# Performance work log

Hardware: AMD Instinct MI355X
Metric: run time of the kernel (lower is better)

## Reference

```python
import jax, jax.numpy as jnp
import numpy as np

SHAPE = (64, 64, 64, 16)
RANK = 8


def tr_to_matrix(factors, in_dim):
    # Tensor-ring reconstruction: T[i1..id] = trace(G1[:,i1,:] @ ... @ Gd[:,id,:])
    acc = factors[0]  # (r, n0, r)
    for f in factors[1:]:
        r = acc.shape[0]
        acc = jnp.einsum('amb,bnc->amnc', acc, f).reshape(r, -1, r)
    # close the ring with a trace over the boundary rank
    full = jnp.trace(acc, axis1=0, axis2=2)  # (prod(SHAPE),)
    return full.reshape(in_dim, -1)


def setup_inputs() -> dict:
    key = jax.random.key(0)
    ks = jax.random.split(key, 5)
    x = jax.random.normal(ks[0], (8192, 2048), dtype=jnp.float32)
    factors = {}
    for i, n in enumerate(SHAPE):
        factors[f'f{i}'] = jax.random.uniform(
            ks[i + 1], (RANK, n, RANK), dtype=jnp.float32, minval=-0.1, maxval=0.1)
    return {'x': x, **factors}


def reference(x, f0, f1, f2, f3):
    W = tr_to_matrix([f0, f1, f2, f3], x.shape[1])  # (2048, 2048)
    return jnp.matmul(x, W)
```

## Files before the change

kernel.cpp:

```cpp
#include <hip/hip_runtime.h>
#include <hip/hip_bf16.h>
#include <stdint.h>

typedef unsigned short u16;
typedef __attribute__((ext_vector_type(8))) unsigned short u16x8;
typedef __attribute__((ext_vector_type(8))) __bf16 bf16x8;
typedef __attribute__((ext_vector_type(4))) float f32x4;

__device__ __forceinline__ u16 f2bf(float f) {
    uint32_t u = __builtin_bit_cast(uint32_t, f);
    u = (u + 0x7fffu + ((u >> 16) & 1u)) >> 16;
    return (u16)u;
}

__device__ __forceinline__ float bf2f(u16 v) {
    return __builtin_bit_cast(float, (uint32_t)v << 16);
}

__device__ __forceinline__ bf16x8 cvt8(const float* p) {
    f32x4 a = *(const f32x4*)p;
    f32x4 b = *(const f32x4*)(p + 4);
    u16x8 o;
    o[0] = f2bf(a[0]); o[1] = f2bf(a[1]); o[2] = f2bf(a[2]); o[3] = f2bf(a[3]);
    o[4] = f2bf(b[0]); o[5] = f2bf(b[1]); o[6] = f2bf(b[2]); o[7] = f2bf(b[3]);
    return __builtin_bit_cast(bf16x8, o);
}

__global__ __launch_bounds__(256) void prep_kernel(const float* __restrict__ f0,
                                                   const float* __restrict__ f1,
                                                   const float* __restrict__ f2,
                                                   const float* __restrict__ f3,
                                                   u16* __restrict__ H12bT,
                                                   u16* __restrict__ H34T) {
    int gid = blockIdx.x * 256 + threadIdx.x;
    if (gid < 262144) {
        int rc = gid >> 11;
        int k  = gid & 2047;
        int p = rc >> 6, e = rc & 63;
        int a = e >> 3, b = e & 7;
        int i1 = k >> 5, i2 = ((k & 31) << 1) | p;
        float s = 0.f;
#pragma unroll
        for (int m = 0; m < 8; m++)
            s += f0[a * 512 + i1 * 8 + m] * f1[m * 512 + i2 * 8 + b];
        H12bT[gid] = f2bf(s);
    } else {
        int g = gid - 262144;
        int c = g >> 6;
        int e = g & 63;
        int a = e >> 3, b = e & 7;
        int i3 = c >> 4, i4 = c & 15;
        float s = 0.f;
#pragma unroll
        for (int cc = 0; cc < 8; cc++)
            s += f2[b * 512 + i3 * 8 + cc] * f3[cc * 128 + i4 * 8 + a];
        H34T[c * 64 + e] = f2bf(s);
    }
}

__global__ __launch_bounds__(256) void k1_kernel(const float* __restrict__ x,
                                                 const u16* __restrict__ H12bT,
                                                 u16* __restrict__ Ypb) {
    int tid = threadIdx.x, lane = tid & 63, w = tid >> 6;
    int lm = lane & 15, lkE = (lane >> 4) << 3;
    int r0 = blockIdx.x * 128 + w * 32;
    int k0 = blockIdx.y * 256;

    f32x4 acc[2][8];
#pragma unroll
    for (int i = 0; i < 2; ++i)
#pragma unroll
        for (int j = 0; j < 8; ++j) acc[i][j] = (f32x4){0.f, 0.f, 0.f, 0.f};

    const float* xA0 = x + (size_t)(r0 + lm) * 2048 + k0 + lkE;
    const float* xA1 = xA0 + (size_t)16 * 2048;
    const u16*   bP  = H12bT + (size_t)lm * 2048 + k0 + lkE;

#pragma unroll
    for (int kc = 0; kc < 8; ++kc) {
        int ko = kc * 32;
        bf16x8 a0 = cvt8(xA0 + ko);
        bf16x8 a1 = cvt8(xA1 + ko);
        bf16x8 bf[8];
#pragma unroll
        for (int j = 0; j < 8; ++j)
            bf[j] = __builtin_bit_cast(bf16x8, *(const u16x8*)(bP + (size_t)j * 16 * 2048 + ko));
#pragma unroll
        for (int j = 0; j < 8; ++j) {
            acc[0][j] = __builtin_amdgcn_mfma_f32_16x16x32_bf16(a0, bf[j], acc[0][j], 0, 0, 0);
            acc[1][j] = __builtin_amdgcn_mfma_f32_16x16x32_bf16(a1, bf[j], acc[1][j], 0, 0, 0);
        }
    }
    u16* yw = Ypb + (size_t)blockIdx.y * 1048576 + (size_t)(r0 + ((lane >> 4) << 2)) * 128 + lm;
#pragma unroll
    for (int mi = 0; mi < 2; ++mi)
#pragma unroll
        for (int j = 0; j < 8; ++j) {
            f32x4 v = acc[mi][j];
#pragma unroll
            for (int r = 0; r < 4; ++r)
                yw[(size_t)(mi * 16 + r) * 128 + j * 16] = f2bf(v[r]);
        }
}

__global__ __launch_bounds__(256) void k2r_kernel(const u16* __restrict__ Ypb,
                                                  const u16* __restrict__ H34T,
                                                  float* __restrict__ out) {
    __shared__ u16 Yl[32][136];
    int tid = threadIdx.x, lane = tid & 63, w = tid >> 6;
    int lm = lane & 15, lkE = (lane >> 4) << 3;
    int r0 = blockIdx.x * 32;

    {
        int row0 = tid >> 4;
        int ce = (tid & 15) << 3;
        float s0[8], s1[8];
#pragma unroll
        for (int e = 0; e < 8; ++e) { s0[e] = 0.f; s1[e] = 0.f; }
#pragma unroll
        for (int ks = 0; ks < 8; ++ks) {
            const u16* b = Ypb + (size_t)ks * 1048576 + (size_t)r0 * 128;
            u16x8 v0 = *(const u16x8*)(b + (size_t)row0 * 128 + ce);
            u16x8 v1 = *(const u16x8*)(b + (size_t)(16 + row0) * 128 + ce);
#pragma unroll
            for (int e = 0; e < 8; ++e) { s0[e] += bf2f(v0[e]); s1[e] += bf2f(v1[e]); }
        }
        u16x8 o0, o1;
#pragma unroll
        for (int e = 0; e < 8; ++e) { o0[e] = f2bf(s0[e]); o1[e] = f2bf(s1[e]); }
        *(u16x8*)&Yl[row0][ce] = o0;
        *(u16x8*)&Yl[16 + row0][ce] = o1;
    }
    __syncthreads();

    int p = w >> 1, ch = (w & 1) << 9;
    bf16x8 ya[2][2];
#pragma unroll
    for (int rh = 0; rh < 2; ++rh)
#pragma unroll
        for (int kc = 0; kc < 2; ++kc)
            ya[rh][kc] = __builtin_bit_cast(bf16x8,
                *(const u16x8*)&Yl[rh * 16 + lm][p * 64 + kc * 32 + lkE]);

    const u16* hB = H34T + (size_t)(ch + lm) * 64 + lkE;
    float* cW = out + (size_t)(r0 + ((lane >> 4) << 2)) * 2048 + (w << 9) + lm;

#pragma unroll 4
    for (int cf = 0; cf < 32; ++cf) {
        const u16* hr = hB + (size_t)cf * 1024;
        bf16x8 h0 = __builtin_bit_cast(bf16x8, *(const u16x8*)(hr));
        bf16x8 h1 = __builtin_bit_cast(bf16x8, *(const u16x8*)(hr + 32));
        f32x4 a0 = (f32x4){0.f, 0.f, 0.f, 0.f};
        f32x4 a1 = (f32x4){0.f, 0.f, 0.f, 0.f};
        a0 = __builtin_amdgcn_mfma_f32_16x16x32_bf16(ya[0][0], h0, a0, 0, 0, 0);
        a0 = __builtin_amdgcn_mfma_f32_16x16x32_bf16(ya[0][1], h1, a0, 0, 0, 0);
        a1 = __builtin_amdgcn_mfma_f32_16x16x32_bf16(ya[1][0], h0, a1, 0, 0, 0);
        a1 = __builtin_amdgcn_mfma_f32_16x16x32_bf16(ya[1][1], h1, a1, 0, 0, 0);
#pragma unroll
        for (int r = 0; r < 4; ++r) {
            cW[(size_t)r * 2048 + cf * 16] = a0[r];
            cW[(size_t)(16 + r) * 2048 + cf * 16] = a1[r];
        }
    }
}

extern "C" void kernel_launch(void* const* d_in, const int* in_sizes, int n_in,
                              void* d_out, int out_size, void* d_ws, size_t ws_size,
                              hipStream_t stream) {
    const float* x  = (const float*)d_in[0];
    const float* f0 = (const float*)d_in[1];
    const float* f1 = (const float*)d_in[2];
    const float* f2 = (const float*)d_in[3];
    const float* f3 = (const float*)d_in[4];
    float* out = (float*)d_out;

    char* ws = (char*)d_ws;
    u16* H12bT = (u16*)ws;
    u16* H34T  = (u16*)(ws + (512u << 10));
    u16* Ypb   = (u16*)(ws + (1u << 20));
    if (ws_size < ((size_t)18 << 20)) return;

    prep_kernel<<<1280, 256, 0, stream>>>(f0, f1, f2, f3, H12bT, H34T);
    k1_kernel<<<dim3(64, 8), 256, 0, stream>>>(x, H12bT, Ypb);
    k2r_kernel<<<256, 256, 0, stream>>>(Ypb, H34T, out);
}
```

Before: 58.59 us.

## Halve per-wave work in k1 and double threads per block in k2r

k1 now gives each wave 16 rows instead of 32 and launches twice as many blocks, so there are more waves in flight to hide the latency of streaming x. k2r moves to 512-thread blocks: the reduction step loads one row per thread, and each wave covers 256 output columns instead of 512. The cost is less reuse, since each H12 B-fragment load in k1 now feeds one MFMA instead of two, which doubles B-operand traffic.

Result: slower. 66.77 us (+14.0%).

```diff
diff --git a/kernel.cpp b/kernel.cpp
--- a/kernel.cpp
+++ b/kernel.cpp
@@ -63,47 +63,39 @@
                                                  u16* __restrict__ Ypb) {
     int tid = threadIdx.x, lane = tid & 63, w = tid >> 6;
     int lm = lane & 15, lkE = (lane >> 4) << 3;
-    int r0 = blockIdx.x * 128 + w * 32;
+    int r0 = blockIdx.x * 64 + w * 16;
     int k0 = blockIdx.y * 256;
 
-    f32x4 acc[2][8];
+    f32x4 acc[8];
 #pragma unroll
-    for (int i = 0; i < 2; ++i)
-#pragma unroll
-        for (int j = 0; j < 8; ++j) acc[i][j] = (f32x4){0.f, 0.f, 0.f, 0.f};
+    for (int j = 0; j < 8; ++j) acc[j] = (f32x4){0.f, 0.f, 0.f, 0.f};
 
     const float* xA0 = x + (size_t)(r0 + lm) * 2048 + k0 + lkE;
-    const float* xA1 = xA0 + (size_t)16 * 2048;
     const u16*   bP  = H12bT + (size_t)lm * 2048 + k0 + lkE;
 
 #pragma unroll
     for (int kc = 0; kc < 8; ++kc) {
         int ko = kc * 32;
         bf16x8 a0 = cvt8(xA0 + ko);
-        bf16x8 a1 = cvt8(xA1 + ko);
         bf16x8 bf[8];
 #pragma unroll
         for (int j = 0; j < 8; ++j)
             bf[j] = __builtin_bit_cast(bf16x8, *(const u16x8*)(bP + (size_t)j * 16 * 2048 + ko));
 #pragma unroll
-        for (int j = 0; j < 8; ++j) {
-            acc[0][j] = __builtin_amdgcn_mfma_f32_16x16x32_bf16(a0, bf[j], acc[0][j], 0, 0, 0);
-            acc[1][j] = __builtin_amdgcn_mfma_f32_16x16x32_bf16(a1, bf[j], acc[1][j], 0, 0, 0);
-        }
+        for (int j = 0; j < 8; ++j)
+            acc[j] = __builtin_amdgcn_mfma_f32_16x16x32_bf16(a0, bf[j], acc[j], 0, 0, 0);
     }
     u16* yw = Ypb + (size_t)blockIdx.y * 1048576 + (size_t)(r0 + ((lane >> 4) << 2)) * 128 + lm;
 #pragma unroll
-    for (int mi = 0; mi < 2; ++mi)
+    for (int j = 0; j < 8; ++j) {
+        f32x4 v = acc[j];
 #pragma unroll
-        for (int j = 0; j < 8; ++j) {
-            f32x4 v = acc[mi][j];
-#pragma unroll
-            for (int r = 0; r < 4; ++r)
-                yw[(size_t)(mi * 16 + r) * 128 + j * 16] = f2bf(v[r]);
-        }
+        for (int r = 0; r < 4; ++r)
+            yw[(size_t)r * 128 + j * 16] = f2bf(v[r]);
+    }
 }
 
-__global__ __launch_bounds__(256) void k2r_kernel(const u16* __restrict__ Ypb,
+__global__ __launch_bounds__(512) void k2r_kernel(const u16* __restrict__ Ypb,
                                                   const u16* __restrict__ H34T,
                                                   float* __restrict__ out) {
     __shared__ u16 Yl[32][136];
@@ -114,26 +106,24 @@
     {
         int row0 = tid >> 4;
         int ce = (tid & 15) << 3;
-        float s0[8], s1[8];
+        float s0[8];
 #pragma unroll
-        for (int e = 0; e < 8; ++e) { s0[e] = 0.f; s1[e] = 0.f; }
+        for (int e = 0; e < 8; ++e) s0[e] = 0.f;
 #pragma unroll
         for (int ks = 0; ks < 8; ++ks) {
-            const u16* b = Ypb + (size_t)ks * 1048576 + (size_t)r0 * 128;
-            u16x8 v0 = *(const u16x8*)(b + (size_t)row0 * 128 + ce);
-            u16x8 v1 = *(const u16x8*)(b + (size_t)(16 + row0) * 128 + ce);
+            const u16* b = Ypb + (size_t)ks * 1048576 + (size_t)(r0 + row0) * 128 + ce;
+            u16x8 v = *(const u16x8*)b;
 #pragma unroll
-            for (int e = 0; e < 8; ++e) { s0[e] += bf2f(v0[e]); s1[e] += bf2f(v1[e]); }
+            for (int e = 0; e < 8; ++e) s0[e] += bf2f(v[e]);
         }
-        u16x8 o0, o1;
+        u16x8 o;
 #pragma unroll
-        for (int e = 0; e < 8; ++e) { o0[e] = f2bf(s0[e]); o1[e] = f2bf(s1[e]); }
-        *(u16x8*)&Yl[row0][ce] = o0;
-        *(u16x8*)&Yl[16 + row0][ce] = o1;
+        for (int e = 0; e < 8; ++e) o[e] = f2bf(s0[e]);
+        *(u16x8*)&Yl[row0][ce] = o;
     }
     __syncthreads();
 
-    int p = w >> 1, ch = (w & 1) << 9;
+    int p = w >> 2, ch = (w & 3) << 8;
     bf16x8 ya[2][2];
 #pragma unroll
     for (int rh = 0; rh < 2; ++rh)
@@ -143,10 +133,10 @@
                 *(const u16x8*)&Yl[rh * 16 + lm][p * 64 + kc * 32 + lkE]);
 
     const u16* hB = H34T + (size_t)(ch + lm) * 64 + lkE;
-    float* cW = out + (size_t)(r0 + ((lane >> 4) << 2)) * 2048 + (w << 9) + lm;
+    float* cW = out + (size_t)(r0 + ((lane >> 4) << 2)) * 2048 + (w << 8) + lm;
 
 #pragma unroll 4
-    for (int cf = 0; cf < 32; ++cf) {
+    for (int cf = 0; cf < 16; ++cf) {
         const u16* hr = hB + (size_t)cf * 1024;
         bf16x8 h0 = __builtin_bit_cast(bf16x8, *(const u16x8*)(hr));
         bf16x8 h1 = __builtin_bit_cast(bf16x8, *(const u16x8*)(hr + 32));
@@ -181,6 +171,6 @@
     if (ws_size < ((size_t)18 << 20)) return;
 
     prep_kernel<<<1280, 256, 0, stream>>>(f0, f1, f2, f3, H12bT, H34T);
-    k1_kernel<<<dim3(64, 8), 256, 0, stream>>>(x, H12bT, Ypb);
-    k2r_kernel<<<256, 256, 0, stream>>>(Ypb, H34T, out);
+    k1_kernel<<<dim3(128, 8), 256, 0, stream>>>(x, H12bT, Ypb);
+    k2r_kernel<<<256, 512, 0, stream>>>(Ypb, H34T, out);
 }
```
